# Optimization experiments

Measured on AMD Instinct MI355X. Metric: run time of the kernel, lower is better.

The kernel has to match this reference:

```python
import jax, jax.numpy as jnp
import numpy as np

N, E = 50000, 800000
DIN, DH, DOUT = 128, 128, 64


def setup_inputs() -> dict:
    key = jax.random.key(0)
    ks = jax.random.split(key, 18)
    s = 0.05
    inp = {
        "x": jax.random.normal(ks[0], (N, DIN), dtype=jnp.float32),
        "edge_index": jax.random.randint(ks[1], (2, E), 0, N, dtype=jnp.int64),
        # conv1 MLP: Linear(DIN,DH), Linear(DH,DH)
        "c1_w1": jax.random.normal(ks[2], (DIN, DH), dtype=jnp.float32) * s,
        "c1_b1": jax.random.normal(ks[3], (DH,), dtype=jnp.float32) * s,
        "c1_w2": jax.random.normal(ks[4], (DH, DH), dtype=jnp.float32) * s,
        "c1_b2": jax.random.normal(ks[5], (DH,), dtype=jnp.float32) * s,
        # conv2 MLP
        "c2_w1": jax.random.normal(ks[6], (DH, DH), dtype=jnp.float32) * s,
        "c2_b1": jax.random.normal(ks[7], (DH,), dtype=jnp.float32) * s,
        "c2_w2": jax.random.normal(ks[8], (DH, DH), dtype=jnp.float32) * s,
        "c2_b2": jax.random.normal(ks[9], (DH,), dtype=jnp.float32) * s,
        # conv3 MLP
        "c3_w1": jax.random.normal(ks[10], (DH, DH), dtype=jnp.float32) * s,
        "c3_b1": jax.random.normal(ks[11], (DH,), dtype=jnp.float32) * s,
        "c3_w2": jax.random.normal(ks[12], (DH, DH), dtype=jnp.float32) * s,
        "c3_b2": jax.random.normal(ks[13], (DH,), dtype=jnp.float32) * s,
        # output head
        "lin1_w": jax.random.normal(ks[14], (DH, DH), dtype=jnp.float32) * s,
        "lin1_b": jax.random.normal(ks[15], (DH,), dtype=jnp.float32) * s,
        "lin2_w": jax.random.normal(ks[16], (DH, DOUT), dtype=jnp.float32) * s,
        "lin2_b": jax.random.normal(ks[17], (DOUT,), dtype=jnp.float32) * s,
    }
    return inp


def _gin_conv(h, src, dst, w1, b1, w2, b2):
    # PyG GINConv, eps=0: MLP((1+eps)*x + sum_{j->i} x_j)
    agg = jax.ops.segment_sum(h[src], dst, num_segments=h.shape[0])  # [N, D]
    z = h + agg
    z = jax.nn.relu(z @ w1 + b1)
    return jax.nn.relu(z @ w2 + b2)


def reference(x, edge_index, c1_w1, c1_b1, c1_w2, c1_b2,
              c2_w1, c2_b1, c2_w2, c2_b2,
              c3_w1, c3_b1, c3_w2, c3_b2,
              lin1_w, lin1_b, lin2_w, lin2_b):
    src, dst = edge_index[0], edge_index[1]
    h = _gin_conv(x, src, dst, c1_w1, c1_b1, c1_w2, c1_b2)
    h = jax.nn.relu(h)  # redundant after MLP ReLU, but faithful to source
    h = _gin_conv(h, src, dst, c2_w1, c2_b1, c2_w2, c2_b2)
    h = jax.nn.relu(h)
    h = _gin_conv(h, src, dst, c3_w1, c3_b1, c3_w2, c3_b2)
    h = jax.nn.relu(h @ lin1_w + lin1_b)
    return h @ lin2_w + lin2_b  # [N, DOUT]
```

## Files before the change

### kernel.cpp

```cpp
#include <hip/hip_runtime.h>
#include <hip/hip_bf16.h>

typedef __attribute__((ext_vector_type(8))) short bf16x8;
typedef __attribute__((ext_vector_type(4))) float f32x4;

#define DH 128
#define DOUT 64

static __device__ __forceinline__ unsigned short f2bf(float f) {
    __hip_bfloat16 h = __float2bfloat16(f);
    return *(unsigned short*)&h;
}
static __device__ __forceinline__ float2 bfp2f(unsigned int u) {
    float2 r;
    r.x = __uint_as_float(u << 16);
    r.y = __uint_as_float(u & 0xffff0000u);
    return r;
}


struct WPrep {
    const float* src[8];
    unsigned short* dst[8];
};

__global__ void prep_kernel(const float* __restrict__ x, unsigned short* __restrict__ xb,
                            int n4, WPrep p) {
    int id = blockIdx.x * blockDim.x + threadIdx.x;
    if (id < n4) {
        float4 v = ((const float4*)x)[id];
        ushort4 b;
        b.x = f2bf(v.x); b.y = f2bf(v.y); b.z = f2bf(v.z); b.w = f2bf(v.w);
        ((ushort4*)xb)[id] = b;
        return;
    }
    id -= n4;
    int m, off;
    if (id < 7 * 16384) { m = id >> 14; off = id & 16383; }
    else {
        m = 7; off = id - 7 * 16384;
        if (off >= 8192) return;
    }
    int shift = (m == 7) ? 6 : 7;
    int nc = 1 << shift;
    int k = off >> shift;
    int n = off & (nc - 1);
    p.dst[m][n * 128 + k] = f2bf(p.src[m][off]);
}


__global__ void zero_i32(int* __restrict__ p, int n) {
    int i = blockIdx.x * blockDim.x + threadIdx.x;
    if (i < n) p[i] = 0;
}

__global__ void hist_kernel(const int* __restrict__ dst, int* __restrict__ cnt,
                            int* __restrict__ rank, int E, int n) {
    int e = blockIdx.x * blockDim.x + threadIdx.x;
    if (e < E) {
        int d = dst[e];
        if ((unsigned)d < (unsigned)n) rank[e] = atomicAdd(&cnt[d], 1);
    }
}

__global__ void scan1_kernel(const int* __restrict__ cnt, int* __restrict__ row_ptr,
                             int* __restrict__ bsum, int n) {
    __shared__ int s[256];
    int tid = threadIdx.x;
    int i = blockIdx.x * 256 + tid;
    int v = (i < n) ? cnt[i] : 0;
    s[tid] = v;
    __syncthreads();
    for (int off = 1; off < 256; off <<= 1) {
        int t = (tid >= off) ? s[tid - off] : 0;
        __syncthreads();
        s[tid] += t;
        __syncthreads();
    }
    if (i < n) row_ptr[i] = s[tid] - v;
    if (tid == 255) bsum[blockIdx.x] = s[255];
}

__global__ void scan2_kernel(int* __restrict__ bsum, int nb) {
    __shared__ int s[256];
    int tid = threadIdx.x;
    int v = (tid < nb) ? bsum[tid] : 0;
    s[tid] = v;
    __syncthreads();
    for (int off = 1; off < 256; off <<= 1) {
        int t = (tid >= off) ? s[tid - off] : 0;
        __syncthreads();
        s[tid] += t;
        __syncthreads();
    }
    if (tid < nb) bsum[tid] = s[tid] - v;
}

__global__ void scan3_kernel(int* __restrict__ row_ptr, const int* __restrict__ bsum,
                             int n, int E) {
    int i = blockIdx.x * 256 + threadIdx.x;
    if (i < n) row_ptr[i] += bsum[blockIdx.x];
    if (i == 0) row_ptr[n] = E;
}

__global__ void fill_kernel(const int* __restrict__ src, const int* __restrict__ dst,
                            const int* __restrict__ row_ptr, const int* __restrict__ rank,
                            int* __restrict__ esrc, int E, int n) {
    int e = blockIdx.x * blockDim.x + threadIdx.x;
    if (e < E) {
        int d = dst[e];
        if ((unsigned)d < (unsigned)n)
            esrc[row_ptr[d] + rank[e]] = src[e] * 64;
    }
}


template <bool AGG, int NC2, bool OUT_BF16, bool RELU2>
__launch_bounds__(256, 8)
__global__ void layer_kernel(const unsigned short* __restrict__ h,
                             const int* __restrict__ row_ptr,
                             const int* __restrict__ esrc,
                             const unsigned short* __restrict__ W1t,
                             const float* __restrict__ b1,
                             const unsigned short* __restrict__ W2t,
                             const float* __restrict__ b2,
                             void* __restrict__ outp, int M) {
    constexpr int LDA = 128 + 8;
    __shared__ __align__(16) unsigned short As[16][LDA];
    __shared__ __align__(16) unsigned short Zs[16][LDA];

    int tid = threadIdx.x;
    int wave = __builtin_amdgcn_readfirstlane(tid >> 6);
    int lane = tid & 63;
    int row0 = blockIdx.x * 16;

    const unsigned int* hb = (const unsigned int*)h + lane;

    if (AGG) {
        for (int i = 0; i < 4; ++i) {
            int r = wave * 4 + i;
            int node = row0 + r;
            float2 acc = make_float2(0.f, 0.f);
            if (node < M) {
                acc = bfp2f(hb[node * 64]);
                int b = row_ptr[node], e = row_ptr[node + 1];
                int j = b;
                for (; j + 8 <= e; j += 8) {
                    unsigned int v0 = hb[esrc[j + 0]];
                    unsigned int v1 = hb[esrc[j + 1]];
                    unsigned int v2 = hb[esrc[j + 2]];
                    unsigned int v3 = hb[esrc[j + 3]];
                    unsigned int v4 = hb[esrc[j + 4]];
                    unsigned int v5 = hb[esrc[j + 5]];
                    unsigned int v6 = hb[esrc[j + 6]];
                    unsigned int v7 = hb[esrc[j + 7]];
                    float2 f0 = bfp2f(v0), f1 = bfp2f(v1), f2 = bfp2f(v2), f3 = bfp2f(v3);
                    float2 f4 = bfp2f(v4), f5 = bfp2f(v5), f6 = bfp2f(v6), f7 = bfp2f(v7);
                    acc.x += ((f0.x + f1.x) + (f2.x + f3.x)) +
                             ((f4.x + f5.x) + (f6.x + f7.x));
                    acc.y += ((f0.y + f1.y) + (f2.y + f3.y)) +
                             ((f4.y + f5.y) + (f6.y + f7.y));
                }
                for (; j + 2 <= e; j += 2) {
                    unsigned int v0 = hb[esrc[j]];
                    unsigned int v1 = hb[esrc[j + 1]];
                    float2 f0 = bfp2f(v0), f1 = bfp2f(v1);
                    acc.x += f0.x + f1.x;
                    acc.y += f0.y + f1.y;
                }
                for (; j < e; ++j) {
                    float2 f0 = bfp2f(hb[esrc[j]]);
                    acc.x += f0.x;
                    acc.y += f0.y;
                }
            }
            unsigned int pv = (unsigned int)f2bf(acc.x) | ((unsigned int)f2bf(acc.y) << 16);
            *(unsigned int*)&As[r][lane * 2] = pv;
        }
    } else {
        int r = tid >> 4, ch = tid & 15;
        int grow = row0 + r;
        bf16x8 v = {};
        if (grow < M) v = *(const bf16x8*)(h + (size_t)grow * 128 + ch * 8);
        *(bf16x8*)(&As[r][ch * 8]) = v;
    }
    __syncthreads();

    int quad = lane >> 4;
    int l16 = lane & 15;

    bf16x8 af[4];
#pragma unroll
    for (int kt = 0; kt < 4; ++kt)
        af[kt] = *(const bf16x8*)(&As[l16][kt * 32 + quad * 8]);

#pragma unroll
    for (int p = 0; p < 2; ++p) {
        int ncol = (wave * 2 + p) * 16 + l16;
        const unsigned short* wp = W1t + ncol * 128 + quad * 8;
        f32x4 acc = {0.f, 0.f, 0.f, 0.f};
#pragma unroll
        for (int kt = 0; kt < 4; ++kt) {
            bf16x8 bfr = *(const bf16x8*)(wp + kt * 32);
            acc = __builtin_amdgcn_mfma_f32_16x16x32_bf16(af[kt], bfr, acc, 0, 0, 0);
        }
        float bs = b1[ncol];
#pragma unroll
        for (int r = 0; r < 4; ++r) {
            float v = acc[r] + bs;
            if (v < 0.f) v = 0.f;
            Zs[quad * 4 + r][ncol] = f2bf(v);
        }
    }
    __syncthreads();

    bf16x8 zf[4];
#pragma unroll
    for (int kt = 0; kt < 4; ++kt)
        zf[kt] = *(const bf16x8*)(&Zs[l16][kt * 32 + quad * 8]);

    constexpr int PT2 = NC2 / 64;
#pragma unroll
    for (int p = 0; p < PT2; ++p) {
        int ncol = (wave * PT2 + p) * 16 + l16;
        const unsigned short* wp = W2t + ncol * 128 + quad * 8;
        f32x4 acc = {0.f, 0.f, 0.f, 0.f};
#pragma unroll
        for (int kt = 0; kt < 4; ++kt) {
            bf16x8 bfr = *(const bf16x8*)(wp + kt * 32);
            acc = __builtin_amdgcn_mfma_f32_16x16x32_bf16(zf[kt], bfr, acc, 0, 0, 0);
        }
        float bs = b2[ncol];
#pragma unroll
        for (int r = 0; r < 4; ++r) {
            int grow = row0 + quad * 4 + r;
            if (grow < M) {
                float v = acc[r] + bs;
                if (RELU2 && v < 0.f) v = 0.f;
                if (OUT_BF16)
                    ((unsigned short*)outp)[(size_t)grow * NC2 + ncol] = f2bf(v);
                else
                    ((float*)outp)[(size_t)grow * NC2 + ncol] = v;
            }
        }
    }
}


extern "C" void kernel_launch(void* const* d_in, const int* in_sizes, int n_in,
                              void* d_out, int out_size, void* d_ws, size_t ws_size,
                              hipStream_t stream) {
    const float* x = (const float*)d_in[0];
    const int* ei = (const int*)d_in[1];
    int N = in_sizes[0] / DH;
    int E = in_sizes[1] / 2;
    const int* src = ei;
    const int* dstv = ei + E;

    char* ws = (char*)d_ws;
    size_t off = 0;
    auto alloc = [&](size_t bytes) -> void* {
        void* p = ws + off;
        off += (bytes + 255) & ~(size_t)255;
        return p;
    };
    unsigned short* xb = (unsigned short*)alloc((size_t)N * DH * 2);
    unsigned short* hA = (unsigned short*)alloc((size_t)N * DH * 2);
    unsigned short* hB = (unsigned short*)alloc((size_t)N * DH * 2);
    unsigned short* wt[8];
    for (int m = 0; m < 8; ++m) wt[m] = (unsigned short*)alloc(16384 * 2);
    int* cnt     = (int*)alloc((size_t)N * 4);
    int* row_ptr = (int*)alloc((size_t)(N + 1) * 4);
    int* rank    = (int*)alloc((size_t)E * 4);
    int* bsum    = (int*)alloc(256 * 4);
    int* esrc    = (int*)alloc((size_t)E * 4);

    WPrep wp;
    wp.src[0] = (const float*)d_in[2];
    wp.src[1] = (const float*)d_in[4];
    wp.src[2] = (const float*)d_in[6];
    wp.src[3] = (const float*)d_in[8];
    wp.src[4] = (const float*)d_in[10];
    wp.src[5] = (const float*)d_in[12];
    wp.src[6] = (const float*)d_in[14];
    wp.src[7] = (const float*)d_in[16];
    for (int m = 0; m < 8; ++m) wp.dst[m] = wt[m];
    int n4 = N * DH / 4;
    prep_kernel<<<(n4 + 7 * 16384 + 8192 + 255) / 256, 256, 0, stream>>>(x, xb, n4, wp);

    int nb = (N + 255) / 256;
    int eb = (E + 255) / 256;
    zero_i32<<<nb, 256, 0, stream>>>(cnt, N);
    hist_kernel<<<eb, 256, 0, stream>>>(dstv, cnt, rank, E, N);
    scan1_kernel<<<nb, 256, 0, stream>>>(cnt, row_ptr, bsum, N);
    scan2_kernel<<<1, 256, 0, stream>>>(bsum, nb);
    scan3_kernel<<<nb, 256, 0, stream>>>(row_ptr, bsum, N, E);
    fill_kernel<<<eb, 256, 0, stream>>>(src, dstv, row_ptr, rank, esrc, E, N);

    int gb = (N + 15) / 16;

    const float* c1b1 = (const float*)d_in[3];
    const float* c1b2 = (const float*)d_in[5];
    const float* c2b1 = (const float*)d_in[7];
    const float* c2b2 = (const float*)d_in[9];
    const float* c3b1 = (const float*)d_in[11];
    const float* c3b2 = (const float*)d_in[13];
    const float* l1b  = (const float*)d_in[15];
    const float* l2b  = (const float*)d_in[17];

    layer_kernel<true, 128, true, true><<<gb, 256, 0, stream>>>(
        xb, row_ptr, esrc, wt[0], c1b1, wt[1], c1b2, hA, N);
    layer_kernel<true, 128, true, true><<<gb, 256, 0, stream>>>(
        hA, row_ptr, esrc, wt[2], c2b1, wt[3], c2b2, hB, N);
    layer_kernel<true, 128, true, true><<<gb, 256, 0, stream>>>(
        hB, row_ptr, esrc, wt[4], c3b1, wt[5], c3b2, hA, N);
    layer_kernel<false, 64, false, false><<<gb, 256, 0, stream>>>(
        hA, row_ptr, esrc, wt[6], l1b, wt[7], l2b, d_out, N);
}
```

Baseline: 343.5 us.

## Fuse output head into conv3, vectorize gather, merge CSR build kernels

Restructures the gather so each 16-lane group loads a full 256-byte neighbor row with 16-byte loads, with four edges processed in parallel per wave and the partial sums reduced by cross-lane shuffles. The output head MLP is fused into the third conv layer, which removes one launch and one full write and read of the hidden activations. The cnt zeroing is folded into the prep kernel, and scan3 is merged with fill, cutting small kernel launches. The costs are higher register pressure (launch bounds lowered to 6 waves) and imbalance when the four nodes in a wave have very different degrees.

```diff
diff --git a/kernel.cpp b/kernel.cpp
--- a/kernel.cpp
+++ b/kernel.cpp
@@ -11,11 +11,9 @@
     __hip_bfloat16 h = __float2bfloat16(f);
     return *(unsigned short*)&h;
 }
-static __device__ __forceinline__ float2 bfp2f(unsigned int u) {
-    float2 r;
-    r.x = __uint_as_float(u << 16);
-    r.y = __uint_as_float(u & 0xffff0000u);
-    return r;
+static __device__ __forceinline__ void acc2(float& a0, float& a1, unsigned int u) {
+    a0 += __uint_as_float(u << 16);
+    a1 += __uint_as_float(u & 0xffff0000u);
 }
 
 
@@ -25,7 +23,7 @@
 };
 
 __global__ void prep_kernel(const float* __restrict__ x, unsigned short* __restrict__ xb,
-                            int n4, WPrep p) {
+                            int n4, WPrep p, int* __restrict__ cnt, int N_) {
     int id = blockIdx.x * blockDim.x + threadIdx.x;
     if (id < n4) {
         float4 v = ((const float4*)x)[id];
@@ -35,6 +33,8 @@
         return;
     }
     id -= n4;
+    if (id < N_) { cnt[id] = 0; return; }
+    id -= N_;
     int m, off;
     if (id < 7 * 16384) { m = id >> 14; off = id & 16383; }
     else {
@@ -48,11 +48,6 @@
     p.dst[m][n * 128 + k] = f2bf(p.src[m][off]);
 }
 
-
-__global__ void zero_i32(int* __restrict__ p, int n) {
-    int i = blockIdx.x * blockDim.x + threadIdx.x;
-    if (i < n) p[i] = 0;
-}
 
 __global__ void hist_kernel(const int* __restrict__ dst, int* __restrict__ cnt,
                             int* __restrict__ rank, int E, int n) {
@@ -63,7 +58,7 @@
     }
 }
 
-__global__ void scan1_kernel(const int* __restrict__ cnt, int* __restrict__ row_ptr,
+__global__ void scan1_kernel(const int* __restrict__ cnt, int* __restrict__ rp_part,
                              int* __restrict__ bsum, int n) {
     __shared__ int s[256];
     int tid = threadIdx.x;
@@ -77,7 +72,7 @@
         s[tid] += t;
         __syncthreads();
     }
-    if (i < n) row_ptr[i] = s[tid] - v;
+    if (i < n) rp_part[i] = s[tid] - v;
     if (tid == 255) bsum[blockIdx.x] = s[255];
 }
 
@@ -96,27 +91,24 @@
     if (tid < nb) bsum[tid] = s[tid] - v;
 }
 
-__global__ void scan3_kernel(int* __restrict__ row_ptr, const int* __restrict__ bsum,
-                             int n, int E) {
-    int i = blockIdx.x * 256 + threadIdx.x;
-    if (i < n) row_ptr[i] += bsum[blockIdx.x];
-    if (i == 0) row_ptr[n] = E;
-}
-
-__global__ void fill_kernel(const int* __restrict__ src, const int* __restrict__ dst,
-                            const int* __restrict__ row_ptr, const int* __restrict__ rank,
-                            int* __restrict__ esrc, int E, int n) {
-    int e = blockIdx.x * blockDim.x + threadIdx.x;
-    if (e < E) {
-        int d = dst[e];
+__global__ void scan3_fill_kernel(const int* __restrict__ rp_part, const int* __restrict__ bsum,
+                                  int* __restrict__ row_ptr,
+                                  const int* __restrict__ src, const int* __restrict__ dst,
+                                  const int* __restrict__ rank, int* __restrict__ esrc,
+                                  int n, int E) {
+    int gid = blockIdx.x * blockDim.x + threadIdx.x;
+    if (gid < n) row_ptr[gid] = rp_part[gid] + bsum[gid >> 8];
+    else if (gid == n) row_ptr[n] = E;
+    if (gid < E) {
+        int d = dst[gid];
         if ((unsigned)d < (unsigned)n)
-            esrc[row_ptr[d] + rank[e]] = src[e] * 64;
-    }
-}
-
-
-template <bool AGG, int NC2, bool OUT_BF16, bool RELU2>
-__launch_bounds__(256, 8)
+            esrc[rp_part[d] + bsum[d >> 8] + rank[gid]] = src[gid];
+    }
+}
+
+
+template <bool HEAD>
+__launch_bounds__(256, 6)
 __global__ void layer_kernel(const unsigned short* __restrict__ h,
                              const int* __restrict__ row_ptr,
                              const int* __restrict__ esrc,
@@ -124,6 +116,10 @@
                              const float* __restrict__ b1,
                              const unsigned short* __restrict__ W2t,
                              const float* __restrict__ b2,
+                             const unsigned short* __restrict__ W3t,
+                             const float* __restrict__ b3,
+                             const unsigned short* __restrict__ W4t,
+                             const float* __restrict__ b4,
                              void* __restrict__ outp, int M) {
     constexpr int LDA = 128 + 8;
     __shared__ __align__(16) unsigned short As[16][LDA];
@@ -132,57 +128,81 @@
     int tid = threadIdx.x;
     int wave = __builtin_amdgcn_readfirstlane(tid >> 6);
     int lane = tid & 63;
+    int grp = lane >> 4;
+    int c = lane & 15;
     int row0 = blockIdx.x * 16;
-
-    const unsigned int* hb = (const unsigned int*)h + lane;
-
-    if (AGG) {
+    int nodes0 = row0 + wave * 4;
+
+    int b[4], e[4];
+#pragma unroll
+    for (int i = 0; i < 4; ++i) {
+        int nd = nodes0 + i;
+        b[i] = (nd < M) ? row_ptr[nd] : 0;
+        e[i] = (nd < M) ? row_ptr[nd + 1] : 0;
+    }
+    float acc[4][8];
+#pragma unroll
+    for (int i = 0; i < 4; ++i)
+#pragma unroll
+        for (int j = 0; j < 8; ++j) acc[i][j] = 0.f;
+
+    int pos[4];
+#pragma unroll
+    for (int i = 0; i < 4; ++i) pos[i] = b[i] + grp;
+    int itmax = 0;
+#pragma unroll
+    for (int i = 0; i < 4; ++i) {
+        int it = (e[i] - b[i] + 3) >> 2;
+        itmax = it > itmax ? it : itmax;
+    }
+
+    for (int it = 0; it < itmax; ++it) {
+        int idx[4] = {0, 0, 0, 0};
+#pragma unroll
+        for (int i = 0; i < 4; ++i)
+            if (pos[i] < e[i]) idx[i] = esrc[pos[i]];
+        uint4 u[4];
+#pragma unroll
+        for (int i = 0; i < 4; ++i) u[i] = make_uint4(0u, 0u, 0u, 0u);
+#pragma unroll
+        for (int i = 0; i < 4; ++i)
+            if (pos[i] < e[i])
+                u[i] = *((const uint4*)((const char*)h + ((size_t)idx[i] << 8)) + c);
+#pragma unroll
         for (int i = 0; i < 4; ++i) {
-            int r = wave * 4 + i;
-            int node = row0 + r;
-            float2 acc = make_float2(0.f, 0.f);
-            if (node < M) {
-                acc = bfp2f(hb[node * 64]);
-                int b = row_ptr[node], e = row_ptr[node + 1];
-                int j = b;
-                for (; j + 8 <= e; j += 8) {
-                    unsigned int v0 = hb[esrc[j + 0]];
-                    unsigned int v1 = hb[esrc[j + 1]];
-                    unsigned int v2 = hb[esrc[j + 2]];
-                    unsigned int v3 = hb[esrc[j + 3]];
-                    unsigned int v4 = hb[esrc[j + 4]];
-                    unsigned int v5 = hb[esrc[j + 5]];
-                    unsigned int v6 = hb[esrc[j + 6]];
-                    unsigned int v7 = hb[esrc[j + 7]];
-                    float2 f0 = bfp2f(v0), f1 = bfp2f(v1), f2 = bfp2f(v2), f3 = bfp2f(v3);
-                    float2 f4 = bfp2f(v4), f5 = bfp2f(v5), f6 = bfp2f(v6), f7 = bfp2f(v7);
-                    acc.x += ((f0.x + f1.x) + (f2.x + f3.x)) +
-                             ((f4.x + f5.x) + (f6.x + f7.x));
-                    acc.y += ((f0.y + f1.y) + (f2.y + f3.y)) +
-                             ((f4.y + f5.y) + (f6.y + f7.y));
-                }
-                for (; j + 2 <= e; j += 2) {
-                    unsigned int v0 = hb[esrc[j]];
-                    unsigned int v1 = hb[esrc[j + 1]];
-                    float2 f0 = bfp2f(v0), f1 = bfp2f(v1);
-                    acc.x += f0.x + f1.x;
-                    acc.y += f0.y + f1.y;
-                }
-                for (; j < e; ++j) {
-                    float2 f0 = bfp2f(hb[esrc[j]]);
-                    acc.x += f0.x;
-                    acc.y += f0.y;
-                }
-            }
-            unsigned int pv = (unsigned int)f2bf(acc.x) | ((unsigned int)f2bf(acc.y) << 16);
-            *(unsigned int*)&As[r][lane * 2] = pv;
-        }
-    } else {
-        int r = tid >> 4, ch = tid & 15;
-        int grow = row0 + r;
-        bf16x8 v = {};
-        if (grow < M) v = *(const bf16x8*)(h + (size_t)grow * 128 + ch * 8);
-        *(bf16x8*)(&As[r][ch * 8]) = v;
+            acc2(acc[i][0], acc[i][1], u[i].x);
+            acc2(acc[i][2], acc[i][3], u[i].y);
+            acc2(acc[i][4], acc[i][5], u[i].z);
+            acc2(acc[i][6], acc[i][7], u[i].w);
+            pos[i] += 4;
+        }
+    }
+
+#pragma unroll
+    for (int i = 0; i < 4; ++i) {
+        int nd = nodes0 + i;
+#pragma unroll
+        for (int j = 0; j < 8; ++j) {
+            float v = acc[i][j];
+            v += __shfl_xor(v, 16, 64);
+            v += __shfl_xor(v, 32, 64);
+            acc[i][j] = v;
+        }
+        if (nd < M) {
+            uint4 s = *((const uint4*)((const char*)h + ((size_t)nd << 8)) + c);
+            acc2(acc[i][0], acc[i][1], s.x);
+            acc2(acc[i][2], acc[i][3], s.y);
+            acc2(acc[i][4], acc[i][5], s.z);
+            acc2(acc[i][6], acc[i][7], s.w);
+        }
+        if (grp == 0) {
+            uint4 ov;
+            ov.x = (unsigned)f2bf(acc[i][0]) | ((unsigned)f2bf(acc[i][1]) << 16);
+            ov.y = (unsigned)f2bf(acc[i][2]) | ((unsigned)f2bf(acc[i][3]) << 16);
+            ov.z = (unsigned)f2bf(acc[i][4]) | ((unsigned)f2bf(acc[i][5]) << 16);
+            ov.w = (unsigned)f2bf(acc[i][6]) | ((unsigned)f2bf(acc[i][7]) << 16);
+            *(uint4*)(&As[wave * 4 + i][c * 8]) = ov;
+        }
     }
     __syncthreads();
 
@@ -193,21 +213,19 @@
 #pragma unroll
     for (int kt = 0; kt < 4; ++kt)
         af[kt] = *(const bf16x8*)(&As[l16][kt * 32 + quad * 8]);
-
 #pragma unroll
     for (int p = 0; p < 2; ++p) {
         int ncol = (wave * 2 + p) * 16 + l16;
         const unsigned short* wp = W1t + ncol * 128 + quad * 8;
-        f32x4 acc = {0.f, 0.f, 0.f, 0.f};
-#pragma unroll
-        for (int kt = 0; kt < 4; ++kt) {
-            bf16x8 bfr = *(const bf16x8*)(wp + kt * 32);
-            acc = __builtin_amdgcn_mfma_f32_16x16x32_bf16(af[kt], bfr, acc, 0, 0, 0);
-        }
+        f32x4 a = {0.f, 0.f, 0.f, 0.f};
+#pragma unroll
+        for (int kt = 0; kt < 4; ++kt)
+            a = __builtin_amdgcn_mfma_f32_16x16x32_bf16(
+                af[kt], *(const bf16x8*)(wp + kt * 32), a, 0, 0, 0);
         float bs = b1[ncol];
 #pragma unroll
         for (int r = 0; r < 4; ++r) {
-            float v = acc[r] + bs;
+            float v = a[r] + bs;
             if (v < 0.f) v = 0.f;
             Zs[quad * 4 + r][ncol] = f2bf(v);
         }
@@ -218,29 +236,72 @@
 #pragma unroll
     for (int kt = 0; kt < 4; ++kt)
         zf[kt] = *(const bf16x8*)(&Zs[l16][kt * 32 + quad * 8]);
-
-    constexpr int PT2 = NC2 / 64;
-#pragma unroll
-    for (int p = 0; p < PT2; ++p) {
-        int ncol = (wave * PT2 + p) * 16 + l16;
+#pragma unroll
+    for (int p = 0; p < 2; ++p) {
+        int ncol = (wave * 2 + p) * 16 + l16;
         const unsigned short* wp = W2t + ncol * 128 + quad * 8;
-        f32x4 acc = {0.f, 0.f, 0.f, 0.f};
-#pragma unroll
-        for (int kt = 0; kt < 4; ++kt) {
-            bf16x8 bfr = *(const bf16x8*)(wp + kt * 32);
-            acc = __builtin_amdgcn_mfma_f32_16x16x32_bf16(zf[kt], bfr, acc, 0, 0, 0);
-        }
+        f32x4 a = {0.f, 0.f, 0.f, 0.f};
+#pragma unroll
+        for (int kt = 0; kt < 4; ++kt)
+            a = __builtin_amdgcn_mfma_f32_16x16x32_bf16(
+                zf[kt], *(const bf16x8*)(wp + kt * 32), a, 0, 0, 0);
         float bs = b2[ncol];
 #pragma unroll
         for (int r = 0; r < 4; ++r) {
-            int grow = row0 + quad * 4 + r;
-            if (grow < M) {
-                float v = acc[r] + bs;
-                if (RELU2 && v < 0.f) v = 0.f;
-                if (OUT_BF16)
-                    ((unsigned short*)outp)[(size_t)grow * NC2 + ncol] = f2bf(v);
-                else
-                    ((float*)outp)[(size_t)grow * NC2 + ncol] = v;
+            float v = a[r] + bs;
+            if (v < 0.f) v = 0.f;
+            if (HEAD) {
+                As[quad * 4 + r][ncol] = f2bf(v);
+            } else {
+                int grow = row0 + quad * 4 + r;
+                if (grow < M)
+                    ((unsigned short*)outp)[(size_t)grow * 128 + ncol] = f2bf(v);
+            }
+        }
+    }
+
+    if (HEAD) {
+        __syncthreads();
+        bf16x8 hf[4];
+#pragma unroll
+        for (int kt = 0; kt < 4; ++kt)
+            hf[kt] = *(const bf16x8*)(&As[l16][kt * 32 + quad * 8]);
+#pragma unroll
+        for (int p = 0; p < 2; ++p) {
+            int ncol = (wave * 2 + p) * 16 + l16;
+            const unsigned short* wp = W3t + ncol * 128 + quad * 8;
+            f32x4 a = {0.f, 0.f, 0.f, 0.f};
+#pragma unroll
+            for (int kt = 0; kt < 4; ++kt)
+                a = __builtin_amdgcn_mfma_f32_16x16x32_bf16(
+                    hf[kt], *(const bf16x8*)(wp + kt * 32), a, 0, 0, 0);
+            float bs = b3[ncol];
+#pragma unroll
+            for (int r = 0; r < 4; ++r) {
+                float v = a[r] + bs;
+                if (v < 0.f) v = 0.f;
+                Zs[quad * 4 + r][ncol] = f2bf(v);
+            }
+        }
+        __syncthreads();
+        bf16x8 gf[4];
+#pragma unroll
+        for (int kt = 0; kt < 4; ++kt)
+            gf[kt] = *(const bf16x8*)(&Zs[l16][kt * 32 + quad * 8]);
+        {
+            int ncol = wave * 16 + l16;
+            const unsigned short* wp = W4t + ncol * 128 + quad * 8;
+            f32x4 a = {0.f, 0.f, 0.f, 0.f};
+#pragma unroll
+            for (int kt = 0; kt < 4; ++kt)
+                a = __builtin_amdgcn_mfma_f32_16x16x32_bf16(
+                    gf[kt], *(const bf16x8*)(wp + kt * 32), a, 0, 0, 0);
+            float bs = b4[ncol];
+#pragma unroll
+            for (int r = 0; r < 4; ++r) {
+                int grow = row0 + quad * 4 + r;
+                if (grow < M)
+                    ((float*)outp)[(size_t)grow * 64 + ncol] = a[r] + bs;
             }
         }
     }
@@ -270,6 +331,7 @@
     unsigned short* wt[8];
     for (int m = 0; m < 8; ++m) wt[m] = (unsigned short*)alloc(16384 * 2);
     int* cnt     = (int*)alloc((size_t)N * 4);
+    int* rp_part = (int*)alloc((size_t)N * 4);
     int* row_ptr = (int*)alloc((size_t)(N + 1) * 4);
     int* rank    = (int*)alloc((size_t)E * 4);
     int* bsum    = (int*)alloc(256 * 4);
@@ -286,16 +348,16 @@
     wp.src[7] = (const float*)d_in[16];
     for (int m = 0; m < 8; ++m) wp.dst[m] = wt[m];
     int n4 = N * DH / 4;
-    prep_kernel<<<(n4 + 7 * 16384 + 8192 + 255) / 256, 256, 0, stream>>>(x, xb, n4, wp);
+    int prep_items = n4 + N + 7 * 16384 + 8192;
+    prep_kernel<<<(prep_items + 255) / 256, 256, 0, stream>>>(x, xb, n4, wp, cnt, N);
 
     int nb = (N + 255) / 256;
     int eb = (E + 255) / 256;
-    zero_i32<<<nb, 256, 0, stream>>>(cnt, N);
     hist_kernel<<<eb, 256, 0, stream>>>(dstv, cnt, rank, E, N);
-    scan1_kernel<<<nb, 256, 0, stream>>>(cnt, row_ptr, bsum, N);
+    scan1_kernel<<<nb, 256, 0, stream>>>(cnt, rp_part, bsum, N);
     scan2_kernel<<<1, 256, 0, stream>>>(bsum, nb);
-    scan3_kernel<<<nb, 256, 0, stream>>>(row_ptr, bsum, N, E);
-    fill_kernel<<<eb, 256, 0, stream>>>(src, dstv, row_ptr, rank, esrc, E, N);
+    scan3_fill_kernel<<<eb, 256, 0, stream>>>(rp_part, bsum, row_ptr,
+                                              src, dstv, rank, esrc, N, E);
 
     int gb = (N + 15) / 16;
 
@@ -308,12 +370,13 @@
     const float* l1b  = (const float*)d_in[15];
     const float* l2b  = (const float*)d_in[17];
 
-    layer_kernel<true, 128, true, true><<<gb, 256, 0, stream>>>(
-        xb, row_ptr, esrc, wt[0], c1b1, wt[1], c1b2, hA, N);
-    layer_kernel<true, 128, true, true><<<gb, 256, 0, stream>>>(
-        hA, row_ptr, esrc, wt[2], c2b1, wt[3], c2b2, hB, N);
-    layer_kernel<true, 128, true, true><<<gb, 256, 0, stream>>>(
-        hB, row_ptr, esrc, wt[4], c3b1, wt[5], c3b2, hA, N);
-    layer_kernel<false, 64, false, false><<<gb, 256, 0, stream>>>(
-        hA, row_ptr, esrc, wt[6], l1b, wt[7], l2b, d_out, N);
-}
+    layer_kernel<false><<<gb, 256, 0, stream>>>(
+        xb, row_ptr, esrc, wt[0], c1b1, wt[1], c1b2,
+        nullptr, nullptr, nullptr, nullptr, hA, N);
+    layer_kernel<false><<<gb, 256, 0, stream>>>(
+        hA, row_ptr, esrc, wt[2], c2b1, wt[3], c2b2,
+        nullptr, nullptr, nullptr, nullptr, hB, N);
+    layer_kernel<true><<<gb, 256, 0, stream>>>(
+        hB, row_ptr, esrc, wt[4], c3b1, wt[5], c3b2,
+        wt[6], l1b, wt[7], l2b, d_out, N);
+}
```

Result: slower. 364.2 us (+6.0%).
